# Kernel optimization log

Hardware: AMD Instinct MI355X
Metric: run time of the kernel (lower is better)

Reference implementation:

```python
import jax, jax.numpy as jnp
import numpy as np

B, N, F = 2, 100000, 64
E = 800000
E_OUT, N_OUT = 16, 64


def setup_inputs() -> dict:
    key = jax.random.key(0)
    ks = jax.random.split(key, 8)
    x = jax.random.normal(ks[0], (B, N, F), dtype=jnp.float32)
    edge_src = jax.random.randint(ks[1], (E,), 0, N, dtype=jnp.int32)
    edge_target = jax.random.randint(ks[2], (E,), 0, N, dtype=jnp.int32)
    edge_weight = jax.random.uniform(ks[3], (E, 1), dtype=jnp.float32)
    in_dim = 2 * F + 1  # 129
    W_e = jax.random.normal(ks[4], (in_dim, E_OUT), dtype=jnp.float32) / np.sqrt(in_dim)
    b_e = jnp.zeros((E_OUT,), dtype=jnp.float32)
    W_n = jax.random.normal(ks[5], (E_OUT, N_OUT), dtype=jnp.float32) / np.sqrt(E_OUT)
    b_n = jnp.zeros((N_OUT,), dtype=jnp.float32)
    return {"x": x, "edge_src": edge_src, "edge_target": edge_target,
            "edge_weight": edge_weight, "W_e": W_e, "b_e": b_e,
            "W_n": W_n, "b_n": b_n}


def reference(x, edge_src, edge_target, edge_weight, W_e, b_e, W_n, b_n):
    # gather endpoint features: [B, E, F]
    node_src = x[:, edge_src]
    node_target = x[:, edge_target]
    # per-edge learned scalar weight broadcast over batch: [B, E, 1]
    ew = jnp.broadcast_to(edge_weight[None, :, :], (x.shape[0], edge_weight.shape[0], 1))
    h = jnp.concatenate([node_src, node_target, ew], axis=-1)  # [B, E, 2F+1]
    h = jax.nn.sigmoid(h @ W_e + b_e)                           # edge MLP -> [B, E, 16]
    # scatter_add(+h at target) + scatter_add(-h at src) -> [B, N, 16]
    agg = jnp.zeros((x.shape[0], x.shape[1], h.shape[-1]), dtype=h.dtype)
    agg = agg.at[:, edge_target].add(h).at[:, edge_src].add(-h)
    out = jax.nn.sigmoid(agg @ W_n + b_n)                       # node MLP -> [B, N, out_dim]
    return out
```

## Files before the change

### kernel.cpp

```cpp
#include <hip/hip_runtime.h>
#include <hip/hip_fp16.h>

#define NB 2
#define NN 100000
#define NF 64
#define NE 800000
#define EO 16
#define NO 64

__device__ __forceinline__ float sigmoidf(float v) {
    return 1.0f / (1.0f + __expf(-v));
}

__global__ __launch_bounds__(256) void pre_kernel(
    const float* __restrict__ x, const float* __restrict__ We,
    const float* __restrict__ be, __half* __restrict__ P1h,
    __half* __restrict__ P2h, float4* __restrict__ aggz)
{
    int u = blockIdx.x * 256 + threadIdx.x;
    if (u >= NB * NN) return;
    int b = u >= NN;
    int n = u - b * NN;

    if (!b) {
        float4 z = make_float4(0.f, 0.f, 0.f, 0.f);
#pragma unroll
        for (int q = 0; q < 4; ++q) aggz[(size_t)n * 4 + q] = z;
    }

    float a1[EO], a2[EO];
#pragma unroll
    for (int k = 0; k < EO; ++k) { a1[k] = 0.f; a2[k] = be[k]; }

    const float* row = x + (size_t)u * NF;
#pragma unroll 4
    for (int j4 = 0; j4 < 16; ++j4) {
        float4 v = *(const float4*)(row + 4 * j4);
        const float* w1 = We + (size_t)(4 * j4) * EO;
        const float* w2 = We + (size_t)(NF + 4 * j4) * EO;
#pragma unroll
        for (int jj = 0; jj < 4; ++jj) {
            float vv = ((const float*)&v)[jj];
#pragma unroll
            for (int k = 0; k < EO; ++k) {
                a1[k] += vv * w1[jj * EO + k];
                a2[k] += vv * w2[jj * EO + k];
            }
        }
    }

    __half2 h1[8], h2[8];
#pragma unroll
    for (int i = 0; i < 8; ++i) {
        h1[i] = __floats2half2_rn(a1[2 * i], a1[2 * i + 1]);
        h2[i] = __floats2half2_rn(a2[2 * i], a2[2 * i + 1]);
    }
    __half* p1 = P1h + (size_t)n * (NB * EO) + b * EO;
    __half* p2 = P2h + (size_t)n * (NB * EO) + b * EO;
    *(float4*)(p1)     = ((float4*)h1)[0];
    *(float4*)(p1 + 8) = ((float4*)h1)[1];
    *(float4*)(p2)     = ((float4*)h2)[0];
    *(float4*)(p2 + 8) = ((float4*)h2)[1];
}

__global__ __launch_bounds__(256) void edge_kernel(
    const int* __restrict__ esrc, const int* __restrict__ etgt,
    const float* __restrict__ ew, const __half* __restrict__ P1h,
    const __half* __restrict__ P2h, const float* __restrict__ We,
    __half2* __restrict__ agg)
{
    __shared__ __half2 hbuf[256 * 17];
    __shared__ int snode[256];
    __shared__ int tnode[256];

    int tid = threadIdx.x;
    int e = blockIdx.x * 256 + tid;
    int s = esrc[e];
    int t = etgt[e];
    float w = ew[e];
    snode[tid] = s;
    tnode[tid] = t;

    const float* wr = We + (size_t)2 * NF * EO;

    float4 sv[4], tv[4];
    const float4* p1 = (const float4*)(P1h + (size_t)s * (NB * EO));
    const float4* p2 = (const float4*)(P2h + (size_t)t * (NB * EO));
#pragma unroll
    for (int i = 0; i < 4; ++i) { sv[i] = p1[i]; tv[i] = p2[i]; }

    const __half2* sh = (const __half2*)sv;
    const __half2* th = (const __half2*)tv;
    float hs[NB * EO];
#pragma unroll
    for (int i = 0; i < 16; ++i) {
        float2 fs = __half22float2(sh[i]);
        float2 ft = __half22float2(th[i]);
        hs[2 * i]     = sigmoidf(fs.x + ft.x + w * wr[(2 * i) & 15]);
        hs[2 * i + 1] = sigmoidf(fs.y + ft.y + w * wr[(2 * i + 1) & 15]);
    }
#pragma unroll
    for (int j = 0; j < NB * EO / 2; ++j)
        hbuf[tid * 17 + j] = __floats2half2_rn(hs[2 * j], hs[2 * j + 1]);
    __syncthreads();

    int g = tid >> 4;
    int k16 = tid & 15;
#pragma unroll
    for (int i = 0; i < 16; ++i) {
        int el = g + (i << 4);
        __half2 v = hbuf[el * 17 + k16];
        int tt = tnode[el];
        int ss = snode[el];
        unsafeAtomicAdd(agg + (size_t)tt * 16 + k16, v);
        unsafeAtomicAdd(agg + (size_t)ss * 16 + k16, __hneg2(v));
    }
}

__global__ __launch_bounds__(256) void node_kernel(
    const float4* __restrict__ agg4, const float* __restrict__ Wn,
    const float* __restrict__ bn, float* __restrict__ out)
{
    __shared__ float wn[EO * NO];
    int tid = threadIdx.x;
    *(float4*)(wn + tid * 4) = ((const float4*)Wn)[tid];
    __syncthreads();

    int u = blockIdx.x * 256 + tid;
    int row = u >> 4;
    int q = u & 15;
    int b = row >= NN;
    int n = row - b * NN;

    const float4* ar = agg4 + ((size_t)n * NB + b) * 2;
    float4 rr0 = ar[0];
    float4 rr1 = ar[1];
    const __half2* hh0 = (const __half2*)&rr0;
    const __half2* hh1 = (const __half2*)&rr1;
    float a[EO];
#pragma unroll
    for (int i = 0; i < 4; ++i) {
        float2 f0 = __half22float2(hh0[i]);
        float2 f1 = __half22float2(hh1[i]);
        a[2 * i]         = f0.x;
        a[2 * i + 1]     = f0.y;
        a[8 + 2 * i]     = f1.x;
        a[8 + 2 * i + 1] = f1.y;
    }

    float4 acc = *(const float4*)(bn + q * 4);
#pragma unroll
    for (int k = 0; k < EO; ++k) {
        float ak = a[k];
        float4 wv = *(const float4*)(wn + k * NO + q * 4);
        acc.x += ak * wv.x;
        acc.y += ak * wv.y;
        acc.z += ak * wv.z;
        acc.w += ak * wv.w;
    }
    float4 o = make_float4(sigmoidf(acc.x), sigmoidf(acc.y),
                           sigmoidf(acc.z), sigmoidf(acc.w));
    *(float4*)(out + (size_t)row * NO + q * 4) = o;
}

extern "C" void kernel_launch(void* const* d_in, const int* in_sizes, int n_in,
                              void* d_out, int out_size, void* d_ws, size_t ws_size,
                              hipStream_t stream) {
    const float* x    = (const float*)d_in[0];
    const int*   esrc = (const int*)d_in[1];
    const int*   etgt = (const int*)d_in[2];
    const float* ew   = (const float*)d_in[3];
    const float* We   = (const float*)d_in[4];
    const float* be   = (const float*)d_in[5];
    const float* Wn   = (const float*)d_in[6];
    const float* bn   = (const float*)d_in[7];
    float* out = (float*)d_out;

    __half2* agg = (__half2*)d_ws;
    __half* P1h = (__half*)((char*)d_ws + (size_t)NN * NB * EO * sizeof(__half));
    __half* P2h = P1h + (size_t)NN * NB * EO;

    pre_kernel<<<(NB * NN + 255) / 256, 256, 0, stream>>>(x, We, be, P1h, P2h,
                                                          (float4*)agg);
    edge_kernel<<<NE / 256, 256, 0, stream>>>(esrc, etgt, ew, P1h, P2h, We, agg);
    node_kernel<<<NB * NN * 16 / 256, 256, 0, stream>>>((const float4*)agg, Wn,
                                                        bn, out);
}
```

Before: 232.8 us.

## Replace packed fp16 atomics with 64-bit fixed-point packed integer atomics

Edge outputs are quantized to 16-bit fixed point (scale 512) and packed four per 64-bit word. The scatter then needs half as many atomic operations, using integer 64-bit atomicAdd instead of half2 atomics. The node kernel decodes the lanes with carry-aware sign extension and folds the 1/512 scale into the node weights. This relies on per-node sums staying inside the int16 range and adds quantization error in place of fp16 rounding.

```diff
diff --git a/kernel.cpp b/kernel.cpp
--- a/kernel.cpp
+++ b/kernel.cpp
@@ -7,6 +7,7 @@
 #define NE 800000
 #define EO 16
 #define NO 64
+#define QS 512.0f
 
 __device__ __forceinline__ float sigmoidf(float v) {
     return 1.0f / (1.0f + __expf(-v));
@@ -67,9 +68,9 @@
     const int* __restrict__ esrc, const int* __restrict__ etgt,
     const float* __restrict__ ew, const __half* __restrict__ P1h,
     const __half* __restrict__ P2h, const float* __restrict__ We,
-    __half2* __restrict__ agg)
+    unsigned long long* __restrict__ agg)
 {
-    __shared__ __half2 hbuf[256 * 17];
+    __shared__ unsigned long long hbuf[256 * 9];
     __shared__ int snode[256];
     __shared__ int tnode[256];
 
@@ -99,31 +100,43 @@
         hs[2 * i]     = sigmoidf(fs.x + ft.x + w * wr[(2 * i) & 15]);
         hs[2 * i + 1] = sigmoidf(fs.y + ft.y + w * wr[(2 * i + 1) & 15]);
     }
-#pragma unroll
-    for (int j = 0; j < NB * EO / 2; ++j)
-        hbuf[tid * 17 + j] = __floats2half2_rn(hs[2 * j], hs[2 * j + 1]);
+
+#pragma unroll
+    for (int j = 0; j < 8; ++j) {
+        long long q0 = __float2int_rn(hs[4 * j + 0] * QS);
+        long long q1 = __float2int_rn(hs[4 * j + 1] * QS);
+        long long q2 = __float2int_rn(hs[4 * j + 2] * QS);
+        long long q3 = __float2int_rn(hs[4 * j + 3] * QS);
+        hbuf[tid * 9 + j] =
+            (unsigned long long)(q0 + (q1 << 16) + (q2 << 32) + (q3 << 48));
+    }
     __syncthreads();
 
-    int g = tid >> 4;
-    int k16 = tid & 15;
-#pragma unroll
-    for (int i = 0; i < 16; ++i) {
-        int el = g + (i << 4);
-        __half2 v = hbuf[el * 17 + k16];
+    int g = tid >> 3;
+    int k8 = tid & 7;
+#pragma unroll
+    for (int i = 0; i < 8; ++i) {
+        int el = g + (i << 5);
+        unsigned long long v = hbuf[el * 9 + k8];
         int tt = tnode[el];
         int ss = snode[el];
-        unsafeAtomicAdd(agg + (size_t)tt * 16 + k16, v);
-        unsafeAtomicAdd(agg + (size_t)ss * 16 + k16, __hneg2(v));
+        atomicAdd(agg + (size_t)tt * 8 + k8, v);
+        atomicAdd(agg + (size_t)ss * 8 + k8, 0ULL - v);
     }
 }
 
 __global__ __launch_bounds__(256) void node_kernel(
-    const float4* __restrict__ agg4, const float* __restrict__ Wn,
+    const unsigned long long* __restrict__ agg, const float* __restrict__ Wn,
     const float* __restrict__ bn, float* __restrict__ out)
 {
     __shared__ float wn[EO * NO];
     int tid = threadIdx.x;
-    *(float4*)(wn + tid * 4) = ((const float4*)Wn)[tid];
+    {
+        float4 wv = ((const float4*)Wn)[tid];
+        wv.x *= (1.0f / QS); wv.y *= (1.0f / QS);
+        wv.z *= (1.0f / QS); wv.w *= (1.0f / QS);
+        *(float4*)(wn + tid * 4) = wv;
+    }
     __syncthreads();
 
     int u = blockIdx.x * 256 + tid;
@@ -132,20 +145,26 @@
     int b = row >= NN;
     int n = row - b * NN;
 
-    const float4* ar = agg4 + ((size_t)n * NB + b) * 2;
-    float4 rr0 = ar[0];
-    float4 rr1 = ar[1];
-    const __half2* hh0 = (const __half2*)&rr0;
-    const __half2* hh1 = (const __half2*)&rr1;
+    const unsigned long long* ar = agg + ((size_t)n * NB + b) * 4;
+    ulonglong2 w01 = ((const ulonglong2*)ar)[0];
+    ulonglong2 w23 = ((const ulonglong2*)ar)[1];
+    unsigned long long ww[4] = { w01.x, w01.y, w23.x, w23.y };
+
     float a[EO];
 #pragma unroll
-    for (int i = 0; i < 4; ++i) {
-        float2 f0 = __half22float2(hh0[i]);
-        float2 f1 = __half22float2(hh1[i]);
-        a[2 * i]         = f0.x;
-        a[2 * i + 1]     = f0.y;
-        a[8 + 2 * i]     = f1.x;
-        a[8 + 2 * i + 1] = f1.y;
+    for (int j = 0; j < 4; ++j) {
+        unsigned long long wv = ww[j];
+        int s0 = (short)(unsigned short)wv;
+        wv = (wv - (unsigned long long)(long long)s0) >> 16;
+        int s1 = (short)(unsigned short)wv;
+        wv = (wv - (unsigned long long)(long long)s1) >> 16;
+        int s2 = (short)(unsigned short)wv;
+        wv = (wv - (unsigned long long)(long long)s2) >> 16;
+        int s3 = (short)(unsigned short)wv;
+        a[4 * j + 0] = (float)s0;
+        a[4 * j + 1] = (float)s1;
+        a[4 * j + 2] = (float)s2;
+        a[4 * j + 3] = (float)s3;
     }
 
     float4 acc = *(const float4*)(bn + q * 4);
@@ -176,13 +195,12 @@
     const float* bn   = (const float*)d_in[7];
     float* out = (float*)d_out;
 
-    __half2* agg = (__half2*)d_ws;
-    __half* P1h = (__half*)((char*)d_ws + (size_t)NN * NB * EO * sizeof(__half));
+    unsigned long long* agg = (unsigned long long*)d_ws;
+    __half* P1h = (__half*)((char*)d_ws + (size_t)NN * 8 * sizeof(unsigned long long));
     __half* P2h = P1h + (size_t)NN * NB * EO;
 
     pre_kernel<<<(NB * NN + 255) / 256, 256, 0, stream>>>(x, We, be, P1h, P2h,
                                                           (float4*)agg);
     edge_kernel<<<NE / 256, 256, 0, stream>>>(esrc, etgt, ew, P1h, P2h, We, agg);
-    node_kernel<<<NB * NN * 16 / 256, 256, 0, stream>>>((const float4*)agg, Wn,
-                                                        bn, out);
-}
+    node_kernel<<<NB * NN * 16 / 256, 256, 0, stream>>>(agg, Wn, bn, out);
+}
```

Result: faster. 223.1 us (-4.2%).
